# Optimization experiments

Measured on AMD Instinct MI355X. Metric: run time of the kernel, lower is better.

Reference implementation:

```python
import jax, jax.numpy as jnp
import numpy as np

NUM_TOKENS = 1024
EMBED_DIM = 64
BETA = 1.0


def setup_inputs() -> dict:
    key = jax.random.key(0)
    k_z, k_cb = jax.random.split(key)
    z = jax.random.normal(k_z, (32, 2048, EMBED_DIM), dtype=jnp.float32)
    bound = 1.0 / NUM_TOKENS
    codebook = jax.random.uniform(
        k_cb, (NUM_TOKENS, EMBED_DIM), dtype=jnp.float32,
        minval=-bound, maxval=bound)
    return {"z": z, "codebook": codebook}


def reference(z, codebook):
    B, T, D = z.shape
    f = z.reshape(-1, D)  # [N, D]
    # squared L2 distances to each code: ||f||^2 - 2 f.c + ||c||^2  -> [N, K]
    dist = ((f ** 2).sum(axis=1, keepdims=True)
            - 2.0 * f @ codebook.T
            + (codebook ** 2).sum(axis=1))
    idx = jnp.argmin(dist, axis=-1)  # [N]
    z_q = codebook[idx].reshape(B, T, D)
    c_loss = BETA * jnp.mean((jax.lax.stop_gradient(z) - z_q) ** 2)
    cb_loss = jnp.mean((z - jax.lax.stop_gradient(z_q)) ** 2)
    z_q_out = z + jax.lax.stop_gradient(z_q - z)  # straight-through
    return (z_q_out, c_loss, cb_loss)
```

## Files before the change

kernel.cpp:

```cpp
#include <hip/hip_runtime.h>


#define VQ_NTOK   65536
#define VQ_D      64
#define VQ_K      1024
#define VQ_NELEM  (VQ_NTOK * VQ_D)

typedef short bf16x8 __attribute__((ext_vector_type(8)));
typedef float f32x4  __attribute__((ext_vector_type(4)));

#define WS_CSQ       0
#define WS_LOSS      1024
#define WS_CBB_BYTES 8192

__device__ __forceinline__ short bf16rn(float x) {
    unsigned u = __builtin_bit_cast(unsigned, x);
    u += 0x7fffu + ((u >> 16) & 1u);
    return (short)(u >> 16);
}

__global__ __launch_bounds__(256) void vq_prep(const float* __restrict__ cb,
                                               float* __restrict__ ws) {
    int t = blockIdx.x * 256 + threadIdx.x;
    if (t == 0) ws[WS_LOSS] = 0.0f;
    if (t < VQ_K) {
        const float4* row = (const float4*)(cb + t * VQ_D);
        float s = 0.f;
        #pragma unroll
        for (int j = 0; j < 16; ++j) {
            float4 c = row[j];
            s += c.x * c.x + c.y * c.y + c.z * c.z + c.w * c.w;
        }
        ws[WS_CSQ + t] = s;
    }
    int c = t >> 7, h = (t >> 6) & 1, L = t & 63;
    int k  = c * 16 + (L & 15);
    int d0 = h * 32 + ((L >> 4) << 3);
    const float4* p = (const float4*)(cb + k * VQ_D + d0);
    float4 x0 = p[0], x1 = p[1];
    bf16x8 v;
    v[0] = bf16rn(x0.x); v[1] = bf16rn(x0.y); v[2] = bf16rn(x0.z); v[3] = bf16rn(x0.w);
    v[4] = bf16rn(x1.x); v[5] = bf16rn(x1.y); v[6] = bf16rn(x1.z); v[7] = bf16rn(x1.w);
    bf16x8* cbb = (bf16x8*)((char*)ws + WS_CBB_BYTES);
    cbb[(c * 2 + h) * 64 + L] = v;
}

__global__ __launch_bounds__(256, 4) void vq_mfma(
        const float* __restrict__ z, const float* __restrict__ cb,
        float* __restrict__ ws, float* __restrict__ out) {
    const int tid  = threadIdx.x;
    const int lane = tid & 63;
    const int wave = tid >> 6;
    const int m    = lane & 15;
    const int q    = lane >> 4;
    const int tokbase = blockIdx.x << 6;

    __shared__ float s_bv[4][64];
    __shared__ int   s_bk[4][64];
    __shared__ float s_loss[4];

    bf16x8 aA[4][2];
    #pragma unroll
    for (int t = 0; t < 4; ++t) {
        const float* rowp = z + (size_t)(tokbase + t * 16 + m) * VQ_D + (q << 3);
        #pragma unroll
        for (int h = 0; h < 2; ++h) {
            const float4* p = (const float4*)(rowp + h * 32);
            float4 x0 = p[0], x1 = p[1];
            bf16x8 v;
            v[0] = bf16rn(x0.x); v[1] = bf16rn(x0.y); v[2] = bf16rn(x0.z); v[3] = bf16rn(x0.w);
            v[4] = bf16rn(x1.x); v[5] = bf16rn(x1.y); v[6] = bf16rn(x1.z); v[7] = bf16rn(x1.w);
            aA[t][h] = v;
        }
    }

    const bf16x8* cbb = (const bf16x8*)((const char*)ws + WS_CBB_BYTES);
    const float*  csq = ws + WS_CSQ;

    float bestv[4][4]; int bestk[4][4];
    #pragma unroll
    for (int t = 0; t < 4; ++t)
        #pragma unroll
        for (int r = 0; r < 4; ++r) { bestv[t][r] = 3.4e38f; bestk[t][r] = 0; }

    const int c0 = wave << 4;
    for (int cc = 0; cc < 16; ++cc) {
        const int c = c0 + cc;
        bf16x8 b0 = cbb[(c * 2 + 0) * 64 + lane];
        bf16x8 b1 = cbb[(c * 2 + 1) * 64 + lane];
        const float cs    = csq[(c << 4) + m];
        const int   kcode = (c << 4) + m;
        #pragma unroll
        for (int t = 0; t < 4; ++t) {
            f32x4 acc = {0.f, 0.f, 0.f, 0.f};
            acc = __builtin_amdgcn_mfma_f32_16x16x32_bf16(aA[t][0], b0, acc, 0, 0, 0);
            acc = __builtin_amdgcn_mfma_f32_16x16x32_bf16(aA[t][1], b1, acc, 0, 0, 0);
            #pragma unroll
            for (int r = 0; r < 4; ++r) {
                float dist = cs - 2.0f * acc[r];
                if (dist < bestv[t][r]) { bestv[t][r] = dist; bestk[t][r] = kcode; }
            }
        }
    }

    #pragma unroll
    for (int t = 0; t < 4; ++t) {
        #pragma unroll
        for (int r = 0; r < 4; ++r) {
            float v = bestv[t][r]; int k = bestk[t][r];
            #pragma unroll
            for (int off = 1; off < 16; off <<= 1) {
                float v2 = __shfl_xor(v, off);
                int   k2 = __shfl_xor(k, off);
                if (v2 < v || (v2 == v && k2 < k)) { v = v2; k = k2; }
            }
            if (m == 0) {
                int tok = t * 16 + q * 4 + r;
                s_bv[wave][tok] = v; s_bk[wave][tok] = k;
            }
        }
    }
    __syncthreads();

    const int tok = tid >> 2, part = tid & 3;
    float bv = s_bv[0][tok]; int bk = s_bk[0][tok];
    #pragma unroll
    for (int w = 1; w < 4; ++w) {
        float v = s_bv[w][tok]; int k = s_bk[w][tok];
        if (v < bv || (v == bv && k < bk)) { bv = v; bk = k; }
    }
    const float4* crow = (const float4*)(cb + (size_t)bk * VQ_D + part * 16);
    const float4* zrow = (const float4*)(z + (size_t)(tokbase + tok) * VQ_D + part * 16);
    float4*       orow = (float4*)(out + (size_t)(tokbase + tok) * VQ_D + part * 16);
    float lsum = 0.f;
    #pragma unroll
    for (int j = 0; j < 4; ++j) {
        float4 cv = crow[j], zv = zrow[j];
        orow[j] = cv;
        float e0 = zv.x - cv.x, e1 = zv.y - cv.y;
        float e2 = zv.z - cv.z, e3 = zv.w - cv.w;
        lsum += e0 * e0 + e1 * e1 + e2 * e2 + e3 * e3;
    }
    #pragma unroll
    for (int off = 32; off > 0; off >>= 1) lsum += __shfl_down(lsum, off);
    if (lane == 0) s_loss[wave] = lsum;
    __syncthreads();
    if (tid == 0)
        atomicAdd(ws + WS_LOSS, s_loss[0] + s_loss[1] + s_loss[2] + s_loss[3]);
}

__global__ void vq_fin(const float* __restrict__ ws, float* __restrict__ out) {
    if (threadIdx.x == 0 && blockIdx.x == 0) {
        float msq = ws[WS_LOSS] * (1.0f / (float)VQ_NELEM);
        out[VQ_NELEM]     = msq;
        out[VQ_NELEM + 1] = msq;
    }
}

extern "C" void kernel_launch(void* const* d_in, const int* in_sizes, int n_in,
                              void* d_out, int out_size, void* d_ws, size_t ws_size,
                              hipStream_t stream) {
    const float* z  = (const float*)d_in[0];
    const float* cb = (const float*)d_in[1];
    float* out = (float*)d_out;
    float* ws  = (float*)d_ws;

    vq_prep<<<dim3(32), dim3(256), 0, stream>>>(cb, ws);
    vq_mfma<<<dim3(VQ_NTOK / 64), dim3(256), 0, stream>>>(z, cb, ws, out);
    vq_fin<<<dim3(1), dim3(64), 0, stream>>>(ws, out);
}
```

Measured before the change: 106.7 us.

## Pack code index into distance bits, share A loads via LDS, fuse finalize

```diff
diff --git a/kernel.cpp b/kernel.cpp
--- a/kernel.cpp
+++ b/kernel.cpp
@@ -5,12 +5,14 @@
 #define VQ_D      64
 #define VQ_K      1024
 #define VQ_NELEM  (VQ_NTOK * VQ_D)
+#define VQ_BLOCKS (VQ_NTOK / 64)
 
 typedef short bf16x8 __attribute__((ext_vector_type(8)));
 typedef float f32x4  __attribute__((ext_vector_type(4)));
 
-#define WS_CSQ       0
+#define WS_CSQ1      0
 #define WS_LOSS      1024
+#define WS_CTR       1025
 #define WS_CBB_BYTES 8192
 
 __device__ __forceinline__ short bf16rn(float x) {
@@ -22,16 +24,19 @@
 __global__ __launch_bounds__(256) void vq_prep(const float* __restrict__ cb,
                                                float* __restrict__ ws) {
     int t = blockIdx.x * 256 + threadIdx.x;
-    if (t == 0) ws[WS_LOSS] = 0.0f;
+    if (t == 0) {
+        ws[WS_LOSS] = 0.0f;
+        ((unsigned*)ws)[WS_CTR] = 0u;
+    }
     if (t < VQ_K) {
         const float4* row = (const float4*)(cb + t * VQ_D);
-        float s = 0.f;
+        float s = 1.0f;
         #pragma unroll
         for (int j = 0; j < 16; ++j) {
             float4 c = row[j];
             s += c.x * c.x + c.y * c.y + c.z * c.z + c.w * c.w;
         }
-        ws[WS_CSQ + t] = s;
+        ws[WS_CSQ1 + t] = s;
     }
     int c = t >> 7, h = (t >> 6) & 1, L = t & 63;
     int k  = c * 16 + (L & 15);
@@ -55,41 +60,51 @@
     const int q    = lane >> 4;
     const int tokbase = blockIdx.x << 6;
 
-    __shared__ float s_bv[4][64];
-    __shared__ int   s_bk[4][64];
-    __shared__ float s_loss[4];
+    __shared__ bf16x8 s_a[8][64];
+    __shared__ float  s_b[4][64];
+    __shared__ float  s_loss[4];
+
+    {
+        const int L = tid & 63;
+        #pragma unroll
+        for (int gi = 0; gi < 2; ++gi) {
+            const int g = (tid >> 6) + gi * 4;
+            const int t = g >> 1, h = g & 1;
+            const int tok = t * 16 + (L & 15);
+            const int d0  = h * 32 + ((L >> 4) << 3);
+            const float4* p = (const float4*)(z + (size_t)(tokbase + tok) * VQ_D + d0);
+            float4 x0 = p[0], x1 = p[1];
+            bf16x8 v;
+            v[0] = bf16rn(x0.x); v[1] = bf16rn(x0.y); v[2] = bf16rn(x0.z); v[3] = bf16rn(x0.w);
+            v[4] = bf16rn(x1.x); v[5] = bf16rn(x1.y); v[6] = bf16rn(x1.z); v[7] = bf16rn(x1.w);
+            s_a[g][L] = v;
+        }
+    }
+    __syncthreads();
 
     bf16x8 aA[4][2];
     #pragma unroll
     for (int t = 0; t < 4; ++t) {
-        const float* rowp = z + (size_t)(tokbase + t * 16 + m) * VQ_D + (q << 3);
-        #pragma unroll
-        for (int h = 0; h < 2; ++h) {
-            const float4* p = (const float4*)(rowp + h * 32);
-            float4 x0 = p[0], x1 = p[1];
-            bf16x8 v;
-            v[0] = bf16rn(x0.x); v[1] = bf16rn(x0.y); v[2] = bf16rn(x0.z); v[3] = bf16rn(x0.w);
-            v[4] = bf16rn(x1.x); v[5] = bf16rn(x1.y); v[6] = bf16rn(x1.z); v[7] = bf16rn(x1.w);
-            aA[t][h] = v;
-        }
+        aA[t][0] = s_a[t * 2 + 0][lane];
+        aA[t][1] = s_a[t * 2 + 1][lane];
     }
 
-    const bf16x8* cbb = (const bf16x8*)((const char*)ws + WS_CBB_BYTES);
-    const float*  csq = ws + WS_CSQ;
+    const bf16x8* cbb  = (const bf16x8*)((const char*)ws + WS_CBB_BYTES);
+    const float*  csq1 = ws + WS_CSQ1;
 
-    float bestv[4][4]; int bestk[4][4];
+    float bestp[4][4];
     #pragma unroll
     for (int t = 0; t < 4; ++t)
         #pragma unroll
-        for (int r = 0; r < 4; ++r) { bestv[t][r] = 3.4e38f; bestk[t][r] = 0; }
+        for (int r = 0; r < 4; ++r) bestp[t][r] = 3.4e38f;
 
     const int c0 = wave << 4;
     for (int cc = 0; cc < 16; ++cc) {
         const int c = c0 + cc;
         bf16x8 b0 = cbb[(c * 2 + 0) * 64 + lane];
         bf16x8 b1 = cbb[(c * 2 + 1) * 64 + lane];
-        const float cs    = csq[(c << 4) + m];
-        const int   kcode = (c << 4) + m;
+        const float    cs1 = csq1[(c << 4) + m];
+        const unsigned kc  = (unsigned)((c << 4) + m);
         #pragma unroll
         for (int t = 0; t < 4; ++t) {
             f32x4 acc = {0.f, 0.f, 0.f, 0.f};
@@ -97,8 +112,9 @@
             acc = __builtin_amdgcn_mfma_f32_16x16x32_bf16(aA[t][1], b1, acc, 0, 0, 0);
             #pragma unroll
             for (int r = 0; r < 4; ++r) {
-                float dist = cs - 2.0f * acc[r];
-                if (dist < bestv[t][r]) { bestv[t][r] = dist; bestk[t][r] = kcode; }
+                float d = fmaf(-2.0f, acc[r], cs1);
+                unsigned pb = (__builtin_bit_cast(unsigned, d) & 0xFFFFFC00u) | kc;
+                bestp[t][r] = fminf(bestp[t][r], __builtin_bit_cast(float, pb));
             }
         }
     }
@@ -107,28 +123,19 @@
     for (int t = 0; t < 4; ++t) {
         #pragma unroll
         for (int r = 0; r < 4; ++r) {
-            float v = bestv[t][r]; int k = bestk[t][r];
+            float v = bestp[t][r];
             #pragma unroll
-            for (int off = 1; off < 16; off <<= 1) {
-                float v2 = __shfl_xor(v, off);
-                int   k2 = __shfl_xor(k, off);
-                if (v2 < v || (v2 == v && k2 < k)) { v = v2; k = k2; }
-            }
-            if (m == 0) {
-                int tok = t * 16 + q * 4 + r;
-                s_bv[wave][tok] = v; s_bk[wave][tok] = k;
-            }
+            for (int off = 1; off < 16; off <<= 1)
+                v = fminf(v, __shfl_xor(v, off));
+            if (m == 0) s_b[wave][t * 16 + q * 4 + r] = v;
         }
     }
     __syncthreads();
 
     const int tok = tid >> 2, part = tid & 3;
-    float bv = s_bv[0][tok]; int bk = s_bk[0][tok];
-    #pragma unroll
-    for (int w = 1; w < 4; ++w) {
-        float v = s_bv[w][tok]; int k = s_bk[w][tok];
-        if (v < bv || (v == bv && k < bk)) { bv = v; bk = k; }
-    }
+    float pv = fminf(fminf(s_b[0][tok], s_b[1][tok]),
+                     fminf(s_b[2][tok], s_b[3][tok]));
+    const int bk = (int)(__builtin_bit_cast(unsigned, pv) & 1023u);
     const float4* crow = (const float4*)(cb + (size_t)bk * VQ_D + part * 16);
     const float4* zrow = (const float4*)(z + (size_t)(tokbase + tok) * VQ_D + part * 16);
     float4*       orow = (float4*)(out + (size_t)(tokbase + tok) * VQ_D + part * 16);
@@ -145,15 +152,17 @@
     for (int off = 32; off > 0; off >>= 1) lsum += __shfl_down(lsum, off);
     if (lane == 0) s_loss[wave] = lsum;
     __syncthreads();
-    if (tid == 0)
+
+    if (tid == 0) {
         atomicAdd(ws + WS_LOSS, s_loss[0] + s_loss[1] + s_loss[2] + s_loss[3]);
-}
-
-__global__ void vq_fin(const float* __restrict__ ws, float* __restrict__ out) {
-    if (threadIdx.x == 0 && blockIdx.x == 0) {
-        float msq = ws[WS_LOSS] * (1.0f / (float)VQ_NELEM);
-        out[VQ_NELEM]     = msq;
-        out[VQ_NELEM + 1] = msq;
+        __threadfence();
+        unsigned done = atomicAdd((unsigned*)ws + WS_CTR, 1u);
+        if (done == VQ_BLOCKS - 1) {
+            float tot = atomicAdd(ws + WS_LOSS, 0.0f);
+            float msq = tot * (1.0f / (float)VQ_NELEM);
+            out[VQ_NELEM]     = msq;
+            out[VQ_NELEM + 1] = msq;
+        }
     }
 }
 
@@ -166,6 +175,5 @@
     float* ws  = (float*)d_ws;
 
     vq_prep<<<dim3(32), dim3(256), 0, stream>>>(cb, ws);
-    vq_mfma<<<dim3(VQ_NTOK / 64), dim3(256), 0, stream>>>(z, cb, ws, out);
-    vq_fin<<<dim3(1), dim3(64), 0, stream>>>(ws, out);
+    vq_mfma<<<dim3(VQ_BLOCKS), dim3(256), 0, stream>>>(z, cb, ws, out);
 }
```

Measured after the change: 133.8 us. 1.25x slower.
